# Optimization experiments

Hardware: AMD Instinct MI355X
Metric: run time of the kernel (lower is better)

The kernel has to match this reference:

```python
import jax, jax.numpy as jnp
import numpy as np

NUM_HEADS = 16
HEAD_DIM = 64
NEG_INF = -1000000000.0


def rotary_embedding(x, seq_len, head_dim):
    # x: (batch, seq, heads, head_dim)
    positions = jnp.arange(seq_len)
    dim_pairs = jnp.arange(0, head_dim, 2)
    freqs = 1.0 / 10000.0 ** (dim_pairs / head_dim)
    angles = positions[:, None] * freqs[None, :]          # (seq, head_dim/2)
    cos = jnp.cos(angles)[:, None, :]                     # (seq, 1, head_dim/2) -> broadcast over heads
    sin = jnp.sin(angles)[:, None, :]
    x1 = x[..., ::2]
    x2 = x[..., 1::2]
    out1 = x1 * cos - x2 * sin
    out2 = x1 * sin + x2 * cos
    return jnp.stack([out1, out2], axis=-1).reshape(x.shape)


def setup_inputs() -> dict:
    key = jax.random.key(0)
    k1, k2, k3 = jax.random.split(key, 3)
    batch, seq_len, embed_dim = 2, 2048, 1024
    x = jax.random.normal(k1, (batch, seq_len, embed_dim), dtype=jnp.float32)
    W_qkv = jax.random.normal(k2, (embed_dim, 3 * NUM_HEADS * HEAD_DIM), dtype=jnp.float32) * 0.02
    W_out = jax.random.normal(k3, (NUM_HEADS * HEAD_DIM, embed_dim), dtype=jnp.float32) * 0.02
    return {"x": x, "W_qkv": W_qkv, "W_out": W_out}


def reference(x, W_qkv, W_out):
    batch, seq_len, embed_dim = x.shape
    qkv = jnp.einsum('bse,ef->bsf', x, W_qkv)
    qkv = qkv.reshape(batch, seq_len, 3, NUM_HEADS, HEAD_DIM)
    q, k, v = qkv[:, :, 0], qkv[:, :, 1], qkv[:, :, 2]
    q = rotary_embedding(q, seq_len, HEAD_DIM)
    k = rotary_embedding(k, seq_len, HEAD_DIM)
    scale = 1.0 / jnp.sqrt(jnp.asarray(HEAD_DIM, dtype=x.dtype))
    scores = jnp.einsum('bqhd,bkhd->bhqk', q, k) * scale   # (B,H,S,S)
    mask = jnp.tril(jnp.ones((seq_len, seq_len), dtype=bool))[None, None, :, :]
    scores = jnp.where(mask, scores, NEG_INF)
    weights = jax.nn.softmax(scores, axis=-1)
    out = jnp.einsum('bhqk,bkhd->bqhd', weights, v)
    out = out.reshape(batch, seq_len, NUM_HEADS * HEAD_DIM)
    return jnp.einsum('bsf,fe->bse', out, W_out)
```

## Files before the change

kernel.cpp:

```cpp
#include <hip/hip_runtime.h>
#include <hip/hip_bf16.h>

typedef __attribute__((ext_vector_type(8))) short short8;
typedef __attribute__((ext_vector_type(4))) float float4v;

__global__ __launch_bounds__(256) void cvt_f32_bf16(
    const float* __restrict__ in, __hip_bfloat16* __restrict__ out, int n4) {
  const int i = blockIdx.x * 256 + threadIdx.x;
  if (i >= n4) return;
  const float4 v = *(const float4*)(in + (size_t)i * 4);
  __hip_bfloat16 o[4];
  o[0] = __float2bfloat16(v.x); o[1] = __float2bfloat16(v.y);
  o[2] = __float2bfloat16(v.z); o[3] = __float2bfloat16(v.w);
  *(uint2*)(out + (size_t)i * 4) = *(const uint2*)o;
}

__global__ __launch_bounds__(256) void rope_table(float2* __restrict__ tab) {
  const int i = blockIdx.x * 256 + threadIdx.x;
  const int s = i >> 5, p = i & 31;
  const float freq = powf(10000.f, -(float)(p * 2) / 64.f);
  float sn, cs;
  sincosf((float)s * freq, &sn, &cs);
  tab[i] = make_float2(cs, sn);
}

__global__ __launch_bounds__(256) void prep_weights(
    const float* __restrict__ Wqkv, const float* __restrict__ Wout,
    __hip_bfloat16* __restrict__ WqkvT, __hip_bfloat16* __restrict__ WoutT) {
  const int z = blockIdx.z;
  if (z == 1 && blockIdx.x >= 32) return;
  const float* in = z ? Wout : Wqkv;
  __hip_bfloat16* out = z ? WoutT : WqkvT;
  const int R = 1024, C = z ? 1024 : 3072;
  __shared__ __hip_bfloat16 tile[32][33];
  const int c0 = blockIdx.x * 32, r0 = blockIdx.y * 32;
  const int tx = threadIdx.x & 31, ty = threadIdx.x >> 5;
  #pragma unroll
  for (int i = ty; i < 32; i += 8)
    tile[i][tx] = __float2bfloat16(in[(size_t)(r0 + i) * C + (c0 + tx)]);
  __syncthreads();
  #pragma unroll
  for (int i = ty; i < 32; i += 8)
    out[(size_t)(c0 + i) * R + (r0 + tx)] = tile[tx][i];
}

template <typename OutT, int BN>
__global__ __launch_bounds__(256) void gemm_bt(
    const __hip_bfloat16* __restrict__ A,
    const __hip_bfloat16* __restrict__ Bt,
    OutT* __restrict__ C,
    int M, int N, int K) {
  __shared__ __hip_bfloat16 lA[128][64];
  __shared__ __hip_bfloat16 lB[BN][64];
  constexpr int NJ = BN / 32;
  const int t = threadIdx.x;
  const int lane = t & 63, wave = t >> 6;
  const int quad = lane >> 4, ln = lane & 15;
  const int m0 = blockIdx.y * 128, n0 = blockIdx.x * BN;
  const int wm = (wave >> 1) * 64, wn = (wave & 1) * (BN / 2);
  const int srow = lane >> 3;
  const int schunk = ((lane & 7) ^ srow) * 8;

  float4v acc[4][NJ];
  #pragma unroll
  for (int i = 0; i < 4; ++i)
    #pragma unroll
    for (int j = 0; j < NJ; ++j)
      acc[i][j] = (float4v){0.f, 0.f, 0.f, 0.f};

  for (int kt = 0; kt < K; kt += 64) {
    __syncthreads();
    #pragma unroll
    for (int q = 0; q < 4; ++q) {
      const int rbase = wave * 32 + q * 8;
      __builtin_amdgcn_global_load_lds(
          (const __attribute__((address_space(1))) void*)
              (A + (size_t)(m0 + rbase + srow) * K + kt + schunk),
          (__attribute__((address_space(3))) void*)&lA[rbase][0], 16, 0, 0);
    }
    #pragma unroll
    for (int g = 0; g < BN / 32; ++g) {
      const int rbase = wave * (BN / 4) + g * 8;
      __builtin_amdgcn_global_load_lds(
          (const __attribute__((address_space(1))) void*)
              (Bt + (size_t)(n0 + rbase + srow) * K + kt + schunk),
          (__attribute__((address_space(3))) void*)&lB[rbase][0], 16, 0, 0);
    }
    __syncthreads();
    #pragma unroll
    for (int step = 0; step < 2; ++step) {
      short8 af[4], bf[NJ];
      #pragma unroll
      for (int i = 0; i < 4; ++i)
        af[i] = *(const short8*)&lA[wm + i * 16 + ln][((step * 4 + quad) ^ (ln & 7)) * 8];
      #pragma unroll
      for (int j = 0; j < NJ; ++j)
        bf[j] = *(const short8*)&lB[wn + j * 16 + ln][((step * 4 + quad) ^ (ln & 7)) * 8];
      #pragma unroll
      for (int i = 0; i < 4; ++i)
        #pragma unroll
        for (int j = 0; j < NJ; ++j)
          acc[i][j] = __builtin_amdgcn_mfma_f32_16x16x32_bf16(af[i], bf[j], acc[i][j], 0, 0, 0);
    }
  }
  #pragma unroll
  for (int i = 0; i < 4; ++i)
    #pragma unroll
    for (int j = 0; j < NJ; ++j)
      #pragma unroll
      for (int r = 0; r < 4; ++r) {
        const int row = m0 + wm + i * 16 + quad * 4 + r;
        const int col = n0 + wn + j * 16 + ln;
        if constexpr (__is_same(OutT, float))
          C[(size_t)row * N + col] = acc[i][j][r];
        else
          C[(size_t)row * N + col] = __float2bfloat16(acc[i][j][r]);
      }
}

__global__ __launch_bounds__(256) void qkv_prep(
    const __hip_bfloat16* __restrict__ qkv,
    const float2* __restrict__ tab,
    __hip_bfloat16* __restrict__ Q,
    __hip_bfloat16* __restrict__ K,
    __hip_bfloat16* __restrict__ Vt) {
  __shared__ __hip_bfloat16 tile[64][65];
  const int s0 = blockIdx.x * 64;
  const int bh = blockIdx.y;
  const int h = bh & 15, b = bh >> 4;
  const int t = threadIdx.x;

  const int pr = t & 31, sl = t >> 5;
  const int d0 = pr * 2;
  const float qs = 0.125f * 1.44269504088896340736f;
  #pragma unroll
  for (int ss = sl; ss < 64; ss += 8) {
    const int s = s0 + ss;
    const float2 cssn = tab[(size_t)s * 32 + pr];
    const float cs = cssn.x, sn = cssn.y;
    const size_t in_base = (size_t)(b * 2048 + s) * 3072;
    const size_t o = ((size_t)bh * 2048 + s) * 64 + d0;

    __hip_bfloat162 q2 = *(const __hip_bfloat162*)&qkv[in_base + h * 64 + d0];
    float x1 = __bfloat162float(q2.x), x2 = __bfloat162float(q2.y);
    __hip_bfloat162 qo;
    qo.x = __float2bfloat16((x1 * cs - x2 * sn) * qs);
    qo.y = __float2bfloat16((x1 * sn + x2 * cs) * qs);
    *(__hip_bfloat162*)&Q[o] = qo;

    __hip_bfloat162 k2 = *(const __hip_bfloat162*)&qkv[in_base + 1024 + h * 64 + d0];
    x1 = __bfloat162float(k2.x); x2 = __bfloat162float(k2.y);
    __hip_bfloat162 ko;
    ko.x = __float2bfloat16(x1 * cs - x2 * sn);
    ko.y = __float2bfloat16(x1 * sn + x2 * cs);
    *(__hip_bfloat162*)&K[o] = ko;
  }

  const int tx = t & 63, ty = t >> 6;
  #pragma unroll
  for (int i = ty; i < 64; i += 4)
    tile[i][tx] = qkv[(size_t)(b * 2048 + s0 + i) * 3072 + 2048 + h * 64 + tx];
  __syncthreads();
  #pragma unroll
  for (int i = ty; i < 64; i += 4)
    Vt[((size_t)bh * 64 + i) * 2048 + s0 + tx] = tile[tx][i];
}

__global__ __launch_bounds__(256) void attention(
    const __hip_bfloat16* __restrict__ Q,
    const __hip_bfloat16* __restrict__ K,
    const __hip_bfloat16* __restrict__ Vt,
    __hip_bfloat16* __restrict__ attn) {
  __shared__ __hip_bfloat16 lK[2][64][64];
  __shared__ __hip_bfloat16 lV[2][64][64];
  __shared__ __hip_bfloat16 lP[4][16][72];
  const int t = threadIdx.x;
  const int lane = t & 63, w = t >> 6;
  const int quad = lane >> 4, ln = lane & 15;
  const int id = blockIdx.x;
  const int bh = id & 31;
  const int qt = 31 - (id >> 5);
  const int q0 = qt * 64;
  const size_t base = (size_t)bh * 2048 * 64;
  const __hip_bfloat16* Qb = Q + base;
  const __hip_bfloat16* Kb = K + base;
  const __hip_bfloat16* Vb = Vt + base;
  const int b = bh >> 4, h = bh & 15;

  short8 ones;
  #pragma unroll
  for (int i = 0; i < 8; ++i) ones[i] = (short)0x3F80;

  const int srow = lane >> 3;
  const int schunk = ((lane & 7) ^ srow) * 8;
  const int rb0 = w * 16;

  #pragma unroll
  for (int g = 0; g < 2; ++g) {
    const int rbase = rb0 + g * 8;
    __builtin_amdgcn_global_load_lds(
        (const __attribute__((address_space(1))) void*)
            (Kb + (size_t)(rbase + srow) * 64 + schunk),
        (__attribute__((address_space(3))) void*)&lK[0][rbase][0], 16, 0, 0);
    __builtin_amdgcn_global_load_lds(
        (const __attribute__((address_space(1))) void*)
            (Vb + (size_t)(rbase + srow) * 2048 + schunk),
        (__attribute__((address_space(3))) void*)&lV[0][rbase][0], 16, 0, 0);
  }

  short8 qf[2];
  {
    const size_t qrow = (size_t)(q0 + w * 16 + ln) * 64;
    qf[0] = *(const short8*)(Qb + qrow + quad * 8);
    qf[1] = *(const short8*)(Qb + qrow + 32 + quad * 8);
  }

  float4v acc_o[4];
  #pragma unroll
  for (int dt = 0; dt < 4; ++dt) acc_o[dt] = (float4v){0.f, 0.f, 0.f, 0.f};
  float4v acc_l = (float4v){0.f, 0.f, 0.f, 0.f};

  for (int kt = 0; kt <= qt; ++kt) {
    const int buf = kt & 1;
    __syncthreads();

    if (kt < qt) {
      #pragma unroll
      for (int g = 0; g < 2; ++g) {
        const int rbase = rb0 + g * 8;
        __builtin_amdgcn_global_load_lds(
            (const __attribute__((address_space(1))) void*)
                (Kb + (size_t)((kt + 1) * 64 + rbase + srow) * 64 + schunk),
            (__attribute__((address_space(3))) void*)&lK[buf ^ 1][rbase][0], 16, 0, 0);
        __builtin_amdgcn_global_load_lds(
            (const __attribute__((address_space(1))) void*)
                (Vb + (size_t)(rbase + srow) * 2048 + (kt + 1) * 64 + schunk),
            (__attribute__((address_space(3))) void*)&lV[buf ^ 1][rbase][0], 16, 0, 0);
      }
    }

    float4v s4[4];
    #pragma unroll
    for (int nt = 0; nt < 4; ++nt) {
      float4v a = (float4v){0.f, 0.f, 0.f, 0.f};
      #pragma unroll
      for (int step = 0; step < 2; ++step) {
        short8 kf = *(const short8*)&lK[buf][nt * 16 + ln][((step * 4 + quad) ^ (ln & 7)) * 8];
        a = __builtin_amdgcn_mfma_f32_16x16x32_bf16(qf[step], kf, a, 0, 0, 0);
      }
      s4[nt] = a;
    }
    if (kt == qt) {
      #pragma unroll
      for (int nt = 0; nt < 4; ++nt)
        #pragma unroll
        for (int r = 0; r < 4; ++r) {
          const int sk = kt * 64 + nt * 16 + ln;
          const int qr = q0 + w * 16 + quad * 4 + r;
          if (sk > qr) s4[nt][r] = -64.f;
        }
    }
    #pragma unroll
    for (int nt = 0; nt < 4; ++nt)
      #pragma unroll
      for (int r = 0; r < 4; ++r)
        lP[w][quad * 4 + r][nt * 16 + ln] = __float2bfloat16(exp2f(s4[nt][r]));
    #pragma unroll
    for (int step = 0; step < 2; ++step) {
      short8 pf = *(const short8*)&lP[w][ln][step * 32 + quad * 8];
      acc_l = __builtin_amdgcn_mfma_f32_16x16x32_bf16(pf, ones, acc_l, 0, 0, 0);
      #pragma unroll
      for (int dt = 0; dt < 4; ++dt) {
        short8 vf = *(const short8*)&lV[buf][dt * 16 + ln][((step * 4 + quad) ^ (ln & 7)) * 8];
        acc_o[dt] = __builtin_amdgcn_mfma_f32_16x16x32_bf16(pf, vf, acc_o[dt], 0, 0, 0);
      }
    }
  }

  float inv_l[4];
  #pragma unroll
  for (int r = 0; r < 4; ++r) inv_l[r] = 1.0f / acc_l[r];
  #pragma unroll
  for (int dt = 0; dt < 4; ++dt)
    #pragma unroll
    for (int r = 0; r < 4; ++r) {
      const int qr = q0 + w * 16 + quad * 4 + r;
      const size_t rg = (size_t)(b * 2048 + qr);
      const int col = h * 64 + dt * 16 + ln;
      attn[rg * 1024 + col] = __float2bfloat16(acc_o[dt][r] * inv_l[r]);
    }
}

extern "C" void kernel_launch(void* const* d_in, const int* in_sizes, int n_in,
                              void* d_out, int out_size, void* d_ws, size_t ws_size,
                              hipStream_t stream) {
  const float* x    = (const float*)d_in[0];
  const float* Wqkv = (const float*)d_in[1];
  const float* Wout = (const float*)d_in[2];
  float* out = (float*)d_out;

  __hip_bfloat16* ws = (__hip_bfloat16*)d_ws;
  __hip_bfloat16* xb    = ws;
  __hip_bfloat16* WqkvT = xb    + (size_t)4096 * 1024;
  __hip_bfloat16* WoutT = WqkvT + (size_t)3072 * 1024;
  __hip_bfloat16* qkv   = WoutT + (size_t)1024 * 1024;
  __hip_bfloat16* Q     = qkv   + (size_t)4096 * 3072;
  __hip_bfloat16* K     = Q     + (size_t)32 * 2048 * 64;
  __hip_bfloat16* Vt    = K     + (size_t)32 * 2048 * 64;
  __hip_bfloat16* attn  = Vt    + (size_t)32 * 2048 * 64;
  float2*         tab   = (float2*)(attn + (size_t)4096 * 1024);

  cvt_f32_bf16<<<4096, 256, 0, stream>>>(x, xb, 4096 * 1024 / 4);
  rope_table<<<256, 256, 0, stream>>>(tab);
  prep_weights<<<dim3(96, 32, 2), 256, 0, stream>>>(Wqkv, Wout, WqkvT, WoutT);
  gemm_bt<__hip_bfloat16, 128><<<dim3(3072 / 128, 4096 / 128), 256, 0, stream>>>(xb, WqkvT, qkv, 4096, 3072, 1024);
  qkv_prep<<<dim3(32, 32), 256, 0, stream>>>(qkv, tab, Q, K, Vt);
  attention<<<1024, 256, 0, stream>>>(Q, K, Vt, attn);
  gemm_bt<float, 64><<<dim3(1024 / 64, 4096 / 128), 256, 0, stream>>>(attn, WoutT, out, 4096, 1024, 1024);
}
```

Before: 183.3 us.

## Double-buffer GEMM LDS tiles and fuse bf16 conversion with RoPE table kernel

Measured after the change: 190.2 us. +3.8%, slower.

```diff
diff --git a/kernel.cpp b/kernel.cpp
--- a/kernel.cpp
+++ b/kernel.cpp
@@ -4,24 +4,24 @@
 typedef __attribute__((ext_vector_type(8))) short short8;
 typedef __attribute__((ext_vector_type(4))) float float4v;
 
-__global__ __launch_bounds__(256) void cvt_f32_bf16(
-    const float* __restrict__ in, __hip_bfloat16* __restrict__ out, int n4) {
+__global__ __launch_bounds__(256) void cvt_and_table(
+    const float* __restrict__ in, __hip_bfloat16* __restrict__ out,
+    float2* __restrict__ tab) {
+  if (blockIdx.x >= 4096) {
+    const int i = (blockIdx.x - 4096) * 256 + threadIdx.x;
+    const int s = i >> 5, p = i & 31;
+    const float freq = powf(10000.f, -(float)(p * 2) / 64.f);
+    float sn, cs;
+    sincosf((float)s * freq, &sn, &cs);
+    tab[i] = make_float2(cs, sn);
+    return;
+  }
   const int i = blockIdx.x * 256 + threadIdx.x;
-  if (i >= n4) return;
   const float4 v = *(const float4*)(in + (size_t)i * 4);
   __hip_bfloat16 o[4];
   o[0] = __float2bfloat16(v.x); o[1] = __float2bfloat16(v.y);
   o[2] = __float2bfloat16(v.z); o[3] = __float2bfloat16(v.w);
   *(uint2*)(out + (size_t)i * 4) = *(const uint2*)o;
-}
-
-__global__ __launch_bounds__(256) void rope_table(float2* __restrict__ tab) {
-  const int i = blockIdx.x * 256 + threadIdx.x;
-  const int s = i >> 5, p = i & 31;
-  const float freq = powf(10000.f, -(float)(p * 2) / 64.f);
-  float sn, cs;
-  sincosf((float)s * freq, &sn, &cs);
-  tab[i] = make_float2(cs, sn);
 }
 
 __global__ __launch_bounds__(256) void prep_weights(
@@ -50,8 +50,8 @@
     const __hip_bfloat16* __restrict__ Bt,
     OutT* __restrict__ C,
     int M, int N, int K) {
-  __shared__ __hip_bfloat16 lA[128][64];
-  __shared__ __hip_bfloat16 lB[BN][64];
+  __shared__ __hip_bfloat16 lA[2][128][64];
+  __shared__ __hip_bfloat16 lB[2][BN][64];
   constexpr int NJ = BN / 32;
   const int t = threadIdx.x;
   const int lane = t & 63, wave = t >> 6;
@@ -68,34 +68,57 @@
     for (int j = 0; j < NJ; ++j)
       acc[i][j] = (float4v){0.f, 0.f, 0.f, 0.f};
 
-  for (int kt = 0; kt < K; kt += 64) {
+  #pragma unroll
+  for (int q = 0; q < 4; ++q) {
+    const int rbase = wave * 32 + q * 8;
+    __builtin_amdgcn_global_load_lds(
+        (const __attribute__((address_space(1))) void*)
+            (A + (size_t)(m0 + rbase + srow) * K + schunk),
+        (__attribute__((address_space(3))) void*)&lA[0][rbase][0], 16, 0, 0);
+  }
+  #pragma unroll
+  for (int g = 0; g < BN / 32; ++g) {
+    const int rbase = wave * (BN / 4) + g * 8;
+    __builtin_amdgcn_global_load_lds(
+        (const __attribute__((address_space(1))) void*)
+            (Bt + (size_t)(n0 + rbase + srow) * K + schunk),
+        (__attribute__((address_space(3))) void*)&lB[0][rbase][0], 16, 0, 0);
+  }
+
+  const int nk = K >> 6;
+  for (int ki = 0; ki < nk; ++ki) {
+    const int buf = ki & 1;
     __syncthreads();
-    #pragma unroll
-    for (int q = 0; q < 4; ++q) {
-      const int rbase = wave * 32 + q * 8;
-      __builtin_amdgcn_global_load_lds(
-          (const __attribute__((address_space(1))) void*)
-              (A + (size_t)(m0 + rbase + srow) * K + kt + schunk),
-          (__attribute__((address_space(3))) void*)&lA[rbase][0], 16, 0, 0);
-    }
-    #pragma unroll
-    for (int g = 0; g < BN / 32; ++g) {
-      const int rbase = wave * (BN / 4) + g * 8;
-      __builtin_amdgcn_global_load_lds(
-          (const __attribute__((address_space(1))) void*)
-              (Bt + (size_t)(n0 + rbase + srow) * K + kt + schunk),
-          (__attribute__((address_space(3))) void*)&lB[rbase][0], 16, 0, 0);
-    }
-    __syncthreads();
+
+    if (ki + 1 < nk) {
+      const int kn = (ki + 1) << 6;
+      #pragma unroll
+      for (int q = 0; q < 4; ++q) {
+        const int rbase = wave * 32 + q * 8;
+        __builtin_amdgcn_global_load_lds(
+            (const __attribute__((address_space(1))) void*)
+                (A + (size_t)(m0 + rbase + srow) * K + kn + schunk),
+            (__attribute__((address_space(3))) void*)&lA[buf ^ 1][rbase][0], 16, 0, 0);
+      }
+      #pragma unroll
+      for (int g = 0; g < BN / 32; ++g) {
+        const int rbase = wave * (BN / 4) + g * 8;
+        __builtin_amdgcn_global_load_lds(
+            (const __attribute__((address_space(1))) void*)
+                (Bt + (size_t)(n0 + rbase + srow) * K + kn + schunk),
+            (__attribute__((address_space(3))) void*)&lB[buf ^ 1][rbase][0], 16, 0, 0);
+      }
+    }
+
     #pragma unroll
     for (int step = 0; step < 2; ++step) {
       short8 af[4], bf[NJ];
       #pragma unroll
       for (int i = 0; i < 4; ++i)
-        af[i] = *(const short8*)&lA[wm + i * 16 + ln][((step * 4 + quad) ^ (ln & 7)) * 8];
+        af[i] = *(const short8*)&lA[buf][wm + i * 16 + ln][((step * 4 + quad) ^ (ln & 7)) * 8];
       #pragma unroll
       for (int j = 0; j < NJ; ++j)
-        bf[j] = *(const short8*)&lB[wn + j * 16 + ln][((step * 4 + quad) ^ (ln & 7)) * 8];
+        bf[j] = *(const short8*)&lB[buf][wn + j * 16 + ln][((step * 4 + quad) ^ (ln & 7)) * 8];
       #pragma unroll
       for (int i = 0; i < 4; ++i)
         #pragma unroll
@@ -310,8 +333,7 @@
   __hip_bfloat16* attn  = Vt    + (size_t)32 * 2048 * 64;
   float2*         tab   = (float2*)(attn + (size_t)4096 * 1024);
 
-  cvt_f32_bf16<<<4096, 256, 0, stream>>>(x, xb, 4096 * 1024 / 4);
-  rope_table<<<256, 256, 0, stream>>>(tab);
+  cvt_and_table<<<4096 + 256, 256, 0, stream>>>(x, xb, tab);
   prep_weights<<<dim3(96, 32, 2), 256, 0, stream>>>(Wqkv, Wout, WqkvT, WoutT);
   gemm_bt<__hip_bfloat16, 128><<<dim3(3072 / 128, 4096 / 128), 256, 0, stream>>>(xb, WqkvT, qkv, 4096, 3072, 1024);
   qkv_prep<<<dim3(32, 32), 256, 0, stream>>>(qkv, tab, Q, K, Vt);
```

## Fuse RoPE and V transpose into QKV GEMM epilogue, merge cvt with rope table

Applied to the files above, without the earlier changes.

Result: slower. 189.8 us (+3.6%).

```diff
diff --git a/kernel.cpp b/kernel.cpp
--- a/kernel.cpp
+++ b/kernel.cpp
@@ -4,24 +4,24 @@
 typedef __attribute__((ext_vector_type(8))) short short8;
 typedef __attribute__((ext_vector_type(4))) float float4v;
 
-__global__ __launch_bounds__(256) void cvt_f32_bf16(
-    const float* __restrict__ in, __hip_bfloat16* __restrict__ out, int n4) {
+__global__ __launch_bounds__(256) void cvt_and_table(
+    const float* __restrict__ in, __hip_bfloat16* __restrict__ out,
+    float2* __restrict__ tab) {
+  if (blockIdx.x >= 4096) {
+    const int i = (blockIdx.x - 4096) * 256 + threadIdx.x;
+    const int s = i >> 5, p = i & 31;
+    const float freq = powf(10000.f, -(float)(p * 2) / 64.f);
+    float sn, cs;
+    sincosf((float)s * freq, &sn, &cs);
+    tab[i] = make_float2(cs, sn);
+    return;
+  }
   const int i = blockIdx.x * 256 + threadIdx.x;
-  if (i >= n4) return;
   const float4 v = *(const float4*)(in + (size_t)i * 4);
   __hip_bfloat16 o[4];
   o[0] = __float2bfloat16(v.x); o[1] = __float2bfloat16(v.y);
   o[2] = __float2bfloat16(v.z); o[3] = __float2bfloat16(v.w);
   *(uint2*)(out + (size_t)i * 4) = *(const uint2*)o;
-}
-
-__global__ __launch_bounds__(256) void rope_table(float2* __restrict__ tab) {
-  const int i = blockIdx.x * 256 + threadIdx.x;
-  const int s = i >> 5, p = i & 31;
-  const float freq = powf(10000.f, -(float)(p * 2) / 64.f);
-  float sn, cs;
-  sincosf((float)s * freq, &sn, &cs);
-  tab[i] = make_float2(cs, sn);
 }
 
 __global__ __launch_bounds__(256) void prep_weights(
@@ -42,6 +42,105 @@
   #pragma unroll
   for (int i = ty; i < 32; i += 8)
     out[(size_t)(c0 + i) * R + (r0 + tx)] = tile[tx][i];
+}
+
+__global__ __launch_bounds__(256) void gemm_qkv(
+    const __hip_bfloat16* __restrict__ A,
+    const __hip_bfloat16* __restrict__ Bt,
+    const float2* __restrict__ tab,
+    __hip_bfloat16* __restrict__ Q,
+    __hip_bfloat16* __restrict__ K,
+    __hip_bfloat16* __restrict__ Vt) {
+  const int KK = 1024;
+  __shared__ __hip_bfloat16 lA[128][64];
+  __shared__ __hip_bfloat16 lB[128][64];
+  const int t = threadIdx.x;
+  const int lane = t & 63, wave = t >> 6;
+  const int quad = lane >> 4, ln = lane & 15;
+  const int m0 = blockIdx.y * 128, n0 = blockIdx.x * 128;
+  const int wm = (wave >> 1) * 64, wn = (wave & 1) * 64;
+  const int srow = lane >> 3;
+  const int schunk = ((lane & 7) ^ srow) * 8;
+
+  float4v acc[4][4];
+  #pragma unroll
+  for (int i = 0; i < 4; ++i)
+    #pragma unroll
+    for (int j = 0; j < 4; ++j)
+      acc[i][j] = (float4v){0.f, 0.f, 0.f, 0.f};
+
+  for (int kt = 0; kt < KK; kt += 64) {
+    __syncthreads();
+    #pragma unroll
+    for (int q = 0; q < 4; ++q) {
+      const int rbase = wave * 32 + q * 8;
+      __builtin_amdgcn_global_load_lds(
+          (const __attribute__((address_space(1))) void*)
+              (A + (size_t)(m0 + rbase + srow) * KK + kt + schunk),
+          (__attribute__((address_space(3))) void*)&lA[rbase][0], 16, 0, 0);
+      __builtin_amdgcn_global_load_lds(
+          (const __attribute__((address_space(1))) void*)
+              (Bt + (size_t)(n0 + rbase + srow) * KK + kt + schunk),
+          (__attribute__((address_space(3))) void*)&lB[rbase][0], 16, 0, 0);
+    }
+    __syncthreads();
+    #pragma unroll
+    for (int step = 0; step < 2; ++step) {
+      short8 af[4], bf[4];
+      #pragma unroll
+      for (int i = 0; i < 4; ++i)
+        af[i] = *(const short8*)&lA[wm + i * 16 + ln][((step * 4 + quad) ^ (ln & 7)) * 8];
+      #pragma unroll
+      for (int j = 0; j < 4; ++j)
+        bf[j] = *(const short8*)&lB[wn + j * 16 + ln][((step * 4 + quad) ^ (ln & 7)) * 8];
+      #pragma unroll
+      for (int i = 0; i < 4; ++i)
+        #pragma unroll
+        for (int j = 0; j < 4; ++j)
+          acc[i][j] = __builtin_amdgcn_mfma_f32_16x16x32_bf16(af[i], bf[j], acc[i][j], 0, 0, 0);
+    }
+  }
+
+  const int third = n0 >> 10;
+  const int cbase = (n0 & 1023) + wn;
+  const float qs = 0.125f * 1.44269504088896340736f;
+
+  if (third == 2) {
+    #pragma unroll
+    for (int i = 0; i < 4; ++i)
+      #pragma unroll
+      for (int j = 0; j < 4; ++j) {
+        const int c = cbase + j * 16 + ln;
+        const int h = c >> 6, d = c & 63;
+        const int row0 = m0 + wm + i * 16 + quad * 4;
+        const int b = row0 >> 11, s = row0 & 2047;
+        __hip_bfloat16 o4[4];
+        #pragma unroll
+        for (int r = 0; r < 4; ++r) o4[r] = __float2bfloat16(acc[i][j][r]);
+        *(uint2*)&Vt[((size_t)(b * 16 + h) * 64 + d) * 2048 + s] = *(const uint2*)o4;
+      }
+  } else {
+    __hip_bfloat16* O = (third == 0) ? Q : K;
+    #pragma unroll
+    for (int i = 0; i < 4; ++i)
+      #pragma unroll
+      for (int j = 0; j < 4; ++j) {
+        const int c = cbase + j * 16 + ln;
+        const int h = c >> 6, d = c & 63, pr = d >> 1;
+        #pragma unroll
+        for (int r = 0; r < 4; ++r) {
+          const int row = m0 + wm + i * 16 + quad * 4 + r;
+          const int b = row >> 11, s = row & 2047;
+          const float2 t2 = tab[(size_t)s * 32 + pr];
+          const float own = acc[i][j][r];
+          const float oth = __shfl_xor(own, 1);
+          float v = (lane & 1) ? (oth * t2.y + own * t2.x)
+                               : (own * t2.x - oth * t2.y);
+          if (third == 0) v *= qs;
+          O[((size_t)(b * 16 + h) * 2048 + s) * 64 + d] = __float2bfloat16(v);
+        }
+      }
+  }
 }
 
 template <typename OutT, int BN>
@@ -116,54 +215,6 @@
         else
           C[(size_t)row * N + col] = __float2bfloat16(acc[i][j][r]);
       }
-}
-
-__global__ __launch_bounds__(256) void qkv_prep(
-    const __hip_bfloat16* __restrict__ qkv,
-    const float2* __restrict__ tab,
-    __hip_bfloat16* __restrict__ Q,
-    __hip_bfloat16* __restrict__ K,
-    __hip_bfloat16* __restrict__ Vt) {
-  __shared__ __hip_bfloat16 tile[64][65];
-  const int s0 = blockIdx.x * 64;
-  const int bh = blockIdx.y;
-  const int h = bh & 15, b = bh >> 4;
-  const int t = threadIdx.x;
-
-  const int pr = t & 31, sl = t >> 5;
-  const int d0 = pr * 2;
-  const float qs = 0.125f * 1.44269504088896340736f;
-  #pragma unroll
-  for (int ss = sl; ss < 64; ss += 8) {
-    const int s = s0 + ss;
-    const float2 cssn = tab[(size_t)s * 32 + pr];
-    const float cs = cssn.x, sn = cssn.y;
-    const size_t in_base = (size_t)(b * 2048 + s) * 3072;
-    const size_t o = ((size_t)bh * 2048 + s) * 64 + d0;
-
-    __hip_bfloat162 q2 = *(const __hip_bfloat162*)&qkv[in_base + h * 64 + d0];
-    float x1 = __bfloat162float(q2.x), x2 = __bfloat162float(q2.y);
-    __hip_bfloat162 qo;
-    qo.x = __float2bfloat16((x1 * cs - x2 * sn) * qs);
-    qo.y = __float2bfloat16((x1 * sn + x2 * cs) * qs);
-    *(__hip_bfloat162*)&Q[o] = qo;
-
-    __hip_bfloat162 k2 = *(const __hip_bfloat162*)&qkv[in_base + 1024 + h * 64 + d0];
-    x1 = __bfloat162float(k2.x); x2 = __bfloat162float(k2.y);
-    __hip_bfloat162 ko;
-    ko.x = __float2bfloat16(x1 * cs - x2 * sn);
-    ko.y = __float2bfloat16(x1 * sn + x2 * cs);
-    *(__hip_bfloat162*)&K[o] = ko;
-  }
-
-  const int tx = t & 63, ty = t >> 6;
-  #pragma unroll
-  for (int i = ty; i < 64; i += 4)
-    tile[i][tx] = qkv[(size_t)(b * 2048 + s0 + i) * 3072 + 2048 + h * 64 + tx];
-  __syncthreads();
-  #pragma unroll
-  for (int i = ty; i < 64; i += 4)
-    Vt[((size_t)bh * 64 + i) * 2048 + s0 + tx] = tile[tx][i];
 }
 
 __global__ __launch_bounds__(256) void attention(
@@ -303,18 +354,15 @@
   __hip_bfloat16* xb    = ws;
   __hip_bfloat16* WqkvT = xb    + (size_t)4096 * 1024;
   __hip_bfloat16* WoutT = WqkvT + (size_t)3072 * 1024;
-  __hip_bfloat16* qkv   = WoutT + (size_t)1024 * 1024;
-  __hip_bfloat16* Q     = qkv   + (size_t)4096 * 3072;
+  __hip_bfloat16* Q     = WoutT + (size_t)1024 * 1024;
   __hip_bfloat16* K     = Q     + (size_t)32 * 2048 * 64;
   __hip_bfloat16* Vt    = K     + (size_t)32 * 2048 * 64;
   __hip_bfloat16* attn  = Vt    + (size_t)32 * 2048 * 64;
   float2*         tab   = (float2*)(attn + (size_t)4096 * 1024);
 
-  cvt_f32_bf16<<<4096, 256, 0, stream>>>(x, xb, 4096 * 1024 / 4);
-  rope_table<<<256, 256, 0, stream>>>(tab);
+  cvt_and_table<<<4096 + 256, 256, 0, stream>>>(x, xb, tab);
   prep_weights<<<dim3(96, 32, 2), 256, 0, stream>>>(Wqkv, Wout, WqkvT, WoutT);
-  gemm_bt<__hip_bfloat16, 128><<<dim3(3072 / 128, 4096 / 128), 256, 0, stream>>>(xb, WqkvT, qkv, 4096, 3072, 1024);
-  qkv_prep<<<dim3(32, 32), 256, 0, stream>>>(qkv, tab, Q, K, Vt);
+  gemm_qkv<<<dim3(24, 32), 256, 0, stream>>>(xb, WqkvT, tab, Q, K, Vt);
   attention<<<1024, 256, 0, stream>>>(Q, K, Vt, attn);
   gemm_bt<float, 64><<<dim3(1024 / 64, 4096 / 128), 256, 0, stream>>>(attn, WoutT, out, 4096, 1024, 1024);
 }
```
